# Performance work log

Hardware: AMD Instinct MI355X
Metric: run time of the kernel (lower is better)

Reference implementation:

```python
import jax, jax.numpy as jnp
import numpy as np

B, I, C, J, D, H, W = 16, 32, 8, 10, 16, 6, 6
NUM_ROUTING = 3
EPS = 1e-07


def setup_inputs() -> dict:
    key = jax.random.key(0)
    u_hat = jax.random.normal(key, (B, I, C, J, D, H, W), dtype=jnp.float32)
    # torch module fills bias with 0.1, shape (out_capsules, out_channels, 1, 1)
    bias = jnp.full((J, D, 1, 1), 0.1, dtype=jnp.float32)
    return {"u_hat": u_hat, "bias": bias, "num_routing": NUM_ROUTING}


def _squash(s):
    # Faithful to the source: L1 norm over ALL non-batch dims (not per-capsule L2).
    n1 = jnp.sum(jnp.abs(s), axis=(1, 2, 3, 4), keepdims=True)  # [B,1,1,1,1]
    n1_sq = n1 * n1
    return (n1_sq / (1.0 + n1_sq)) * (s / (n1 + EPS))


def reference(u_hat, bias, num_routing):
    # u_hat: [B,I,C,J,D,H,W]; bias: [J,D,1,1]
    b_ij = jnp.zeros((I, J), dtype=u_hat.dtype)
    v_j = None
    for _ in range(num_routing):
        c_ij = jax.nn.softmax(b_ij, axis=1)  # [I,J]
        # s_j[b,j,d,h,w] = sum_{i,c} c[i,j] * u_hat[b,i,c,j,d,h,w]  (c broadcast over in_channels)
        s_j = jnp.einsum('ij,bicjdhw->bjdhw', c_ij, u_hat) + bias
        v_j = _squash(s_j)  # [B,J,D,H,W]
        # agreement[i,j] = sum over b,c,d,h,w of u_hat * v_j (broadcast over i,c)
        agreement = jnp.einsum('bicjdhw,bjdhw->ij', u_hat, v_j)
        b_ij = b_ij + jax.lax.stop_gradient(agreement)  # torch uses .data (detached)
    return v_j
```

## Files before the change

kernel.cpp:

```cpp
#include <hip/hip_runtime.h>


#define NB   16
#define NI   32
#define NC   8
#define NJ   10
#define ND   16
#define NHW  36
#define NDHW 576
#define EPSV 1e-7f

static __device__ __forceinline__ double wave_reduce(double a) {
    #pragma unroll
    for (int off = 32; off > 0; off >>= 1) a += __shfl_down(a, off);
    return a;
}

__global__ __launch_bounds__(256) void reduce_c_kernel(
    const float4* __restrict__ uh, float4* __restrict__ U)
{
    int t = blockIdx.x * 256 + threadIdx.x;
    int f4 = t % 144;
    int j  = (t / 144) % NJ;
    int bi = t / (144 * NJ);
    const float4* p = uh + ((size_t)bi * NC) * (NJ * 144) + j * 144 + f4;
    float4 acc = make_float4(0.f, 0.f, 0.f, 0.f);
    #pragma unroll
    for (int c = 0; c < NC; ++c) {
        float4 v = p[(size_t)c * (NJ * 144)];
        acc.x += v.x; acc.y += v.y; acc.z += v.z; acc.w += v.w;
    }
    U[t] = acc;
}

__global__ __launch_bounds__(NDHW) void s_n1_kernel(
    const float* __restrict__ U, const float* __restrict__ bias,
    const float* __restrict__ b_ij, float* __restrict__ s,
    double* __restrict__ n1)
{
    int blk = blockIdx.x;
    int b = blk / NJ, j = blk - b * NJ;
    int tid = threadIdx.x;

    __shared__ float c_sh[NI];
    if (tid < NI) {
        float row[NJ];
        float m = -1e30f;
        #pragma unroll
        for (int jj = 0; jj < NJ; ++jj) {
            row[jj] = b_ij[tid * NJ + jj];
            m = fmaxf(m, row[jj]);
        }
        float sum = 0.f;
        #pragma unroll
        for (int jj = 0; jj < NJ; ++jj) sum += expf(row[jj] - m);
        c_sh[tid] = expf(row[j] - m) / sum;
    }
    __syncthreads();

    float sv = bias[j * ND + tid / NHW];
    const float* Ub = U + ((size_t)(b * NI) * NJ + j) * NDHW + tid;
    #pragma unroll 8
    for (int i = 0; i < NI; ++i)
        sv += c_sh[i] * Ub[(size_t)i * NJ * NDHW];
    s[((size_t)b * NJ + j) * NDHW + tid] = sv;

    double a = wave_reduce((double)fabsf(sv));
    __shared__ double wpart[NDHW / 64];
    if ((tid & 63) == 0) wpart[tid >> 6] = a;
    __syncthreads();
    if (tid == 0) {
        double t = wpart[0];
        #pragma unroll
        for (int k = 1; k < NDHW / 64; ++k) t += wpart[k];
        atomicAdd(&n1[b], t);
    }
}

__global__ __launch_bounds__(256) void agree_kernel(
    const float* __restrict__ U, const float* __restrict__ s,
    const double* __restrict__ n1, float* __restrict__ b_ij)
{
    int ij = blockIdx.x;
    int i = ij / NJ, j = ij - i * NJ;
    int tid = threadIdx.x;

    __shared__ double sc_sh[NB];
    if (tid < NB) {
        double n1v = n1[tid];
        double nsq = n1v * n1v;
        sc_sh[tid] = (nsq / (1.0 + nsq)) / (n1v + (double)EPSV);
    }
    __syncthreads();

    double acc = 0.0;
    for (int t = tid; t < NB * NDHW; t += 256) {
        int b = t / NDHW, dhw = t - b * NDHW;
        float Uv = U[((size_t)(b * NI + i) * NJ + j) * NDHW + dhw];
        float sv = s[((size_t)b * NJ + j) * NDHW + dhw];
        acc += (double)Uv * (double)sv * sc_sh[b];
    }
    acc = wave_reduce(acc);
    __shared__ double wpart[4];
    if ((tid & 63) == 0) wpart[tid >> 6] = acc;
    __syncthreads();
    if (tid == 0)
        b_ij[i * NJ + j] += (float)(wpart[0] + wpart[1] + wpart[2] + wpart[3]);
}

__global__ __launch_bounds__(256) void vout_kernel(
    const float* __restrict__ s, const double* __restrict__ n1,
    float* __restrict__ out)
{
    int idx = blockIdx.x * 256 + threadIdx.x;
    int b = idx / (NJ * NDHW);
    float n1f = (float)n1[b];
    float nsq = n1f * n1f;
    out[idx] = (nsq / (1.f + nsq)) * (s[idx] / (n1f + EPSV));
}

extern "C" void kernel_launch(void* const* d_in, const int* in_sizes, int n_in,
                              void* d_out, int out_size, void* d_ws, size_t ws_size,
                              hipStream_t stream)
{
    const float* u_hat = (const float*)d_in[0];
    const float* bias  = (const float*)d_in[1];

    float*  U   = (float*)d_ws;
    float*  s   = U + (size_t)NB * NI * NJ * NDHW;
    float*  bij = s + (size_t)NB * NJ * NDHW;
    double* n1  = (double*)(bij + NI * NJ);
    float*  out = (float*)d_out;

    hipMemsetAsync(bij, 0, NI * NJ * sizeof(float) + 3 * NB * sizeof(double), stream);

    reduce_c_kernel<<<(NB * NI * NJ * 144) / 256, 256, 0, stream>>>(
        (const float4*)u_hat, (float4*)U);

    for (int r = 0; r < 3; ++r) {
        s_n1_kernel<<<NB * NJ, NDHW, 0, stream>>>(U, bias, bij, s, n1 + r * NB);
        if (r < 2)
            agree_kernel<<<NI * NJ, 256, 0, stream>>>(U, s, n1 + r * NB, bij);
        else
            vout_kernel<<<(NB * NJ * NDHW) / 256, 256, 0, stream>>>(s, n1 + r * NB, out);
    }
}
```

Measured before the change: 182.4 us.

## Fuse routing iterations into one cooperative kernel with grid syncs

Replaces the six per-iteration launches (s/norm, agreement, output) with a single cooperative kernel of 360 blocks. Grid-wide syncs separate the phases, and the output squash is applied directly from registers. The aim is to remove launch gaps and the extra pass that re-reads s. In exchange it adds grid.sync costs, and it caps parallelism at 360 blocks of 256 threads, since the agreement phase still uses 320 blocks.

```diff
diff --git a/kernel.cpp b/kernel.cpp
--- a/kernel.cpp
+++ b/kernel.cpp
@@ -1,4 +1,7 @@
 #include <hip/hip_runtime.h>
+#include <hip/hip_cooperative_groups.h>
+
+namespace cg = cooperative_groups;
 
 
 #define NB   16
@@ -8,13 +11,11 @@
 #define ND   16
 #define NHW  36
 #define NDHW 576
+#define NJDHW (NJ * NDHW)
+#define NTOT  (NB * NJ * NDHW)
 #define EPSV 1e-7f
-
-static __device__ __forceinline__ double wave_reduce(double a) {
-    #pragma unroll
-    for (int off = 32; off > 0; off >>= 1) a += __shfl_down(a, off);
-    return a;
-}
+#define GRID 360
+#define TPB  256
 
 __global__ __launch_bounds__(256) void reduce_c_kernel(
     const float4* __restrict__ uh, float4* __restrict__ U)
@@ -33,90 +34,107 @@
     U[t] = acc;
 }
 
-__global__ __launch_bounds__(NDHW) void s_n1_kernel(
+__global__ __launch_bounds__(TPB) void routing_kernel(
     const float* __restrict__ U, const float* __restrict__ bias,
-    const float* __restrict__ b_ij, float* __restrict__ s,
-    double* __restrict__ n1)
+    float* __restrict__ s, float* __restrict__ bij,
+    double* __restrict__ n1, float* __restrict__ out)
 {
-    int blk = blockIdx.x;
-    int b = blk / NJ, j = blk - b * NJ;
-    int tid = threadIdx.x;
+    cg::grid_group grid = cg::this_grid();
+    const int tid = threadIdx.x;
+    const int blk = blockIdx.x;
+    const int e   = blk * TPB + tid;
 
-    __shared__ float c_sh[NI];
-    if (tid < NI) {
-        float row[NJ];
-        float m = -1e30f;
+    __shared__ float  c_sh[NI * NJ];
+    __shared__ double red[8];
+    __shared__ double sc_sh[NB];
+
+    const int b   = e / NJDHW;
+    const int rem = e - b * NJDHW;
+    const int j   = rem / NDHW;
+    const int dhw = rem - j * NDHW;
+    const float bias_v = bias[j * ND + dhw / NHW];
+    const float* Up = U + (((size_t)b * NI) * NJ + j) * NDHW + dhw;
+    const int b0 = (blk * TPB) / NJDHW;
+    const int b1 = (blk * TPB + TPB - 1) / NJDHW;
+
+    for (int r = 0; r < 3; ++r) {
+        double* n1r = n1 + r * NB;
+
+        if (tid < NI) {
+            float row[NJ], m = -1e30f;
+            #pragma unroll
+            for (int jj = 0; jj < NJ; ++jj) {
+                row[jj] = bij[tid * NJ + jj];
+                m = fmaxf(m, row[jj]);
+            }
+            float ex[NJ], sum = 0.f;
+            #pragma unroll
+            for (int jj = 0; jj < NJ; ++jj) { ex[jj] = expf(row[jj] - m); sum += ex[jj]; }
+            float inv = 1.f / sum;
+            #pragma unroll
+            for (int jj = 0; jj < NJ; ++jj) c_sh[tid * NJ + jj] = ex[jj] * inv;
+        }
+        __syncthreads();
+
+        float sv = bias_v;
         #pragma unroll
-        for (int jj = 0; jj < NJ; ++jj) {
-            row[jj] = b_ij[tid * NJ + jj];
-            m = fmaxf(m, row[jj]);
+        for (int i = 0; i < NI; ++i)
+            sv += c_sh[i * NJ + j] * Up[(size_t)i * NJ * NDHW];
+        s[e] = sv;
+
+        {
+            double a  = (double)fabsf(sv);
+            double v0 = (b == b0) ? a : 0.0;
+            double v1 = (b1 != b0 && b == b1) ? a : 0.0;
+            #pragma unroll
+            for (int off = 32; off > 0; off >>= 1) {
+                v0 += __shfl_down(v0, off);
+                v1 += __shfl_down(v1, off);
+            }
+            if ((tid & 63) == 0) { red[tid >> 6] = v0; red[4 + (tid >> 6)] = v1; }
+            __syncthreads();
+            if (tid == 0) {
+                atomicAdd(&n1r[b0], red[0] + red[1] + red[2] + red[3]);
+                if (b1 != b0)
+                    atomicAdd(&n1r[b1], red[4] + red[5] + red[6] + red[7]);
+            }
+            __syncthreads();
         }
-        float sum = 0.f;
-        #pragma unroll
-        for (int jj = 0; jj < NJ; ++jj) sum += expf(row[jj] - m);
-        c_sh[tid] = expf(row[j] - m) / sum;
+
+        __threadfence();
+        grid.sync();
+
+        if (r < 2) {
+            if (tid < NB) {
+                double n1v = n1r[tid];
+                double nsq = n1v * n1v;
+                sc_sh[tid] = (nsq / (1.0 + nsq)) / (n1v + (double)EPSV);
+            }
+            __syncthreads();
+            if (blk < NI * NJ) {
+                int ti = blk / NJ, tj = blk - ti * NJ;
+                double acc = 0.0;
+                for (int t = tid; t < NB * NDHW; t += TPB) {
+                    int tb = t / NDHW, tdhw = t - tb * NDHW;
+                    float Uv = U[(((size_t)(tb * NI + ti)) * NJ + tj) * NDHW + tdhw];
+                    float svv = s[(size_t)tb * NJDHW + tj * NDHW + tdhw];
+                    acc += (double)Uv * (double)svv * sc_sh[tb];
+                }
+                #pragma unroll
+                for (int off = 32; off > 0; off >>= 1) acc += __shfl_down(acc, off);
+                if ((tid & 63) == 0) red[tid >> 6] = acc;
+                __syncthreads();
+                if (tid == 0)
+                    bij[blk] += (float)(red[0] + red[1] + red[2] + red[3]);
+            }
+            __threadfence();
+            grid.sync();
+        } else {
+            float n1f = (float)n1r[b];
+            float nsq = n1f * n1f;
+            out[e] = (nsq / (1.f + nsq)) * (sv / (n1f + EPSV));
+        }
     }
-    __syncthreads();
-
-    float sv = bias[j * ND + tid / NHW];
-    const float* Ub = U + ((size_t)(b * NI) * NJ + j) * NDHW + tid;
-    #pragma unroll 8
-    for (int i = 0; i < NI; ++i)
-        sv += c_sh[i] * Ub[(size_t)i * NJ * NDHW];
-    s[((size_t)b * NJ + j) * NDHW + tid] = sv;
-
-    double a = wave_reduce((double)fabsf(sv));
-    __shared__ double wpart[NDHW / 64];
-    if ((tid & 63) == 0) wpart[tid >> 6] = a;
-    __syncthreads();
-    if (tid == 0) {
-        double t = wpart[0];
-        #pragma unroll
-        for (int k = 1; k < NDHW / 64; ++k) t += wpart[k];
-        atomicAdd(&n1[b], t);
-    }
-}
-
-__global__ __launch_bounds__(256) void agree_kernel(
-    const float* __restrict__ U, const float* __restrict__ s,
-    const double* __restrict__ n1, float* __restrict__ b_ij)
-{
-    int ij = blockIdx.x;
-    int i = ij / NJ, j = ij - i * NJ;
-    int tid = threadIdx.x;
-
-    __shared__ double sc_sh[NB];
-    if (tid < NB) {
-        double n1v = n1[tid];
-        double nsq = n1v * n1v;
-        sc_sh[tid] = (nsq / (1.0 + nsq)) / (n1v + (double)EPSV);
-    }
-    __syncthreads();
-
-    double acc = 0.0;
-    for (int t = tid; t < NB * NDHW; t += 256) {
-        int b = t / NDHW, dhw = t - b * NDHW;
-        float Uv = U[((size_t)(b * NI + i) * NJ + j) * NDHW + dhw];
-        float sv = s[((size_t)b * NJ + j) * NDHW + dhw];
-        acc += (double)Uv * (double)sv * sc_sh[b];
-    }
-    acc = wave_reduce(acc);
-    __shared__ double wpart[4];
-    if ((tid & 63) == 0) wpart[tid >> 6] = acc;
-    __syncthreads();
-    if (tid == 0)
-        b_ij[i * NJ + j] += (float)(wpart[0] + wpart[1] + wpart[2] + wpart[3]);
-}
-
-__global__ __launch_bounds__(256) void vout_kernel(
-    const float* __restrict__ s, const double* __restrict__ n1,
-    float* __restrict__ out)
-{
-    int idx = blockIdx.x * 256 + threadIdx.x;
-    int b = idx / (NJ * NDHW);
-    float n1f = (float)n1[b];
-    float nsq = n1f * n1f;
-    out[idx] = (nsq / (1.f + nsq)) * (s[idx] / (n1f + EPSV));
 }
 
 extern "C" void kernel_launch(void* const* d_in, const int* in_sizes, int n_in,
@@ -128,7 +146,7 @@
 
     float*  U   = (float*)d_ws;
     float*  s   = U + (size_t)NB * NI * NJ * NDHW;
-    float*  bij = s + (size_t)NB * NJ * NDHW;
+    float*  bij = s + NTOT;
     double* n1  = (double*)(bij + NI * NJ);
     float*  out = (float*)d_out;
 
@@ -137,11 +155,8 @@
     reduce_c_kernel<<<(NB * NI * NJ * 144) / 256, 256, 0, stream>>>(
         (const float4*)u_hat, (float4*)U);
 
-    for (int r = 0; r < 3; ++r) {
-        s_n1_kernel<<<NB * NJ, NDHW, 0, stream>>>(U, bias, bij, s, n1 + r * NB);
-        if (r < 2)
-            agree_kernel<<<NI * NJ, 256, 0, stream>>>(U, s, n1 + r * NB, bij);
-        else
-            vout_kernel<<<(NB * NJ * NDHW) / 256, 256, 0, stream>>>(s, n1 + r * NB, out);
-    }
+    void* args[] = {(void*)&U, (void*)&bias, (void*)&s, (void*)&bij,
+                    (void*)&n1, (void*)&out};
+    hipLaunchCooperativeKernel((void*)routing_kernel, dim3(GRID), dim3(TPB),
+                               args, 0, stream);
 }
```

Result: slower. 530.9 us (+191.0%).

## Fuse routing iterations into per-(b,j) blocks with unscaled agreement partials

Applied to the files above, without the earlier changes.

Replaces the reduce/s/agree kernel chain with a block per (b,j) that reduces u_hat over C, computes s, its L1 partial and the unscaled per-i dot products G in one pass. Later iterations rebuild b_ij from the stored G partials scaled by each batch's squash factor, so the agree kernel, the atomics and the memset are gone and U is read only once per iteration. Iteration 1 uses uniform coupling (1/10) directly. This costs redundant b_ij/softmax recomputation in every block and 32 wave reductions per block for G, using many registers.

```diff
diff --git a/kernel.cpp b/kernel.cpp
--- a/kernel.cpp
+++ b/kernel.cpp
@@ -8,115 +8,161 @@
 #define ND   16
 #define NHW  36
 #define NDHW 576
+#define NJDHW (NJ * NDHW)
+#define NTOT  (NB * NJ * NDHW)
 #define EPSV 1e-7f
+#define TPB  576
 
-static __device__ __forceinline__ double wave_reduce(double a) {
+
+static __device__ __forceinline__ double wave_sum(double v) {
     #pragma unroll
-    for (int off = 32; off > 0; off >>= 1) a += __shfl_down(a, off);
-    return a;
+    for (int off = 32; off > 0; off >>= 1) v += __shfl_down(v, off);
+    return v;
 }
 
-__global__ __launch_bounds__(256) void reduce_c_kernel(
-    const float4* __restrict__ uh, float4* __restrict__ U)
-{
-    int t = blockIdx.x * 256 + threadIdx.x;
-    int f4 = t % 144;
-    int j  = (t / 144) % NJ;
-    int bi = t / (144 * NJ);
-    const float4* p = uh + ((size_t)bi * NC) * (NJ * 144) + j * 144 + f4;
-    float4 acc = make_float4(0.f, 0.f, 0.f, 0.f);
-    #pragma unroll
-    for (int c = 0; c < NC; ++c) {
-        float4 v = p[(size_t)c * (NJ * 144)];
-        acc.x += v.x; acc.y += v.y; acc.z += v.z; acc.w += v.w;
+static __device__ __forceinline__ void n1_reduce(float sv, double* slot,
+                                                 double* nred ) {
+    int tid = threadIdx.x;
+    double a = wave_sum((double)fabsf(sv));
+    if ((tid & 63) == 0) nred[tid >> 6] = a;
+    __syncthreads();
+    if (tid == 0) {
+        double t = nred[0];
+        #pragma unroll
+        for (int w = 1; w < 9; ++w) t += nred[w];
+        *slot = t;
     }
-    U[t] = acc;
 }
 
-__global__ __launch_bounds__(NDHW) void s_n1_kernel(
-    const float* __restrict__ U, const float* __restrict__ bias,
-    const float* __restrict__ b_ij, float* __restrict__ s,
-    double* __restrict__ n1)
+static __device__ __forceinline__ void g_reduce(const float* Uv, float sv,
+                                                double* gslot,
+                                                double (*gred)[32] ) {
+    int tid = threadIdx.x, w = tid >> 6, lane = tid & 63;
+    #pragma unroll
+    for (int i = 0; i < NI; ++i) {
+        double p = wave_sum((double)Uv[i] * (double)sv);
+        if (lane == 0) gred[w][i] = p;
+    }
+    __syncthreads();
+    if (tid < NI) {
+        double t = gred[0][tid];
+        #pragma unroll
+        for (int w2 = 1; w2 < 9; ++w2) t += gred[w2][tid];
+        gslot[tid] = t;
+    }
+}
+
+__global__ __launch_bounds__(TPB) void a1_kernel(
+    const float* __restrict__ uh, const float* __restrict__ bias,
+    float* __restrict__ U2, double* __restrict__ n1p, double* __restrict__ Gp)
 {
-    int blk = blockIdx.x;
-    int b = blk / NJ, j = blk - b * NJ;
-    int tid = threadIdx.x;
+    __shared__ double nred[9];
+    __shared__ double gred[9][32];
 
-    __shared__ float c_sh[NI];
-    if (tid < NI) {
-        float row[NJ];
-        float m = -1e30f;
+    const int blk = blockIdx.x;
+    const int b = blk / NJ, j = blk - b * NJ;
+    const int tid = threadIdx.x;
+    const float cw = 1.0f / 10.0f;
+
+    const float* ub = uh + (size_t)b * 1474560 + j * 576 + tid;
+    float* u2b = U2 + (size_t)b * 184320 + j * 18432 + tid;
+
+    float Uv[NI];
+    float sv = bias[j * ND + tid / NHW];
+    #pragma unroll 4
+    for (int i = 0; i < NI; ++i) {
+        float acc = 0.f;
         #pragma unroll
-        for (int jj = 0; jj < NJ; ++jj) {
-            row[jj] = b_ij[tid * NJ + jj];
-            m = fmaxf(m, row[jj]);
-        }
-        float sum = 0.f;
+        for (int c = 0; c < NC; ++c)
+            acc += ub[(size_t)i * 46080 + c * 5760];
+        Uv[i] = acc;
+        u2b[i * 576] = acc;
+        sv += cw * acc;
+    }
+
+    n1_reduce(sv, &n1p[b * NJ + j], nred);
+    g_reduce(Uv, sv, &Gp[(size_t)(b * NJ + j) * NI], gred);
+}
+
+template <int R>
+__global__ __launch_bounds__(TPB) void ab_kernel(
+    const float* __restrict__ U2, const float* __restrict__ bias,
+    const double* __restrict__ n1p, double* __restrict__ Gp,
+    double* __restrict__ n1p_out, double* __restrict__ Gp_out,
+    float* __restrict__ s)
+{
+    __shared__ double sc_sh[2][NB];
+    __shared__ float  bij_sh[NI * NJ];
+    __shared__ float  c_sh[NI];
+    __shared__ double nred[9];
+    __shared__ double gred[9][32];
+
+    const int blk = blockIdx.x;
+    const int b = blk / NJ, j = blk - b * NJ;
+    const int tid = threadIdx.x;
+
+    if (tid < R * NB) {
+        int rr = tid / NB, bb = tid - rr * NB;
+        double n1 = 0.0;
         #pragma unroll
-        for (int jj = 0; jj < NJ; ++jj) sum += expf(row[jj] - m);
-        c_sh[tid] = expf(row[j] - m) / sum;
+        for (int jj = 0; jj < NJ; ++jj) n1 += n1p[rr * (NB * NJ) + bb * NJ + jj];
+        double nsq = n1 * n1;
+        sc_sh[rr][bb] = (nsq / (1.0 + nsq)) / (n1 + (double)EPSV);
     }
     __syncthreads();
 
-    float sv = bias[j * ND + tid / NHW];
-    const float* Ub = U + ((size_t)(b * NI) * NJ + j) * NDHW + tid;
-    #pragma unroll 8
-    for (int i = 0; i < NI; ++i)
-        sv += c_sh[i] * Ub[(size_t)i * NJ * NDHW];
-    s[((size_t)b * NJ + j) * NDHW + tid] = sv;
-
-    double a = wave_reduce((double)fabsf(sv));
-    __shared__ double wpart[NDHW / 64];
-    if ((tid & 63) == 0) wpart[tid >> 6] = a;
-    __syncthreads();
-    if (tid == 0) {
-        double t = wpart[0];
+    if (tid < NI * NJ) {
+        int i = tid / NJ, jj = tid - i * NJ;
+        double a = 0.0;
         #pragma unroll
-        for (int k = 1; k < NDHW / 64; ++k) t += wpart[k];
-        atomicAdd(&n1[b], t);
-    }
-}
-
-__global__ __launch_bounds__(256) void agree_kernel(
-    const float* __restrict__ U, const float* __restrict__ s,
-    const double* __restrict__ n1, float* __restrict__ b_ij)
-{
-    int ij = blockIdx.x;
-    int i = ij / NJ, j = ij - i * NJ;
-    int tid = threadIdx.x;
-
-    __shared__ double sc_sh[NB];
-    if (tid < NB) {
-        double n1v = n1[tid];
-        double nsq = n1v * n1v;
-        sc_sh[tid] = (nsq / (1.0 + nsq)) / (n1v + (double)EPSV);
+        for (int rr = 0; rr < R; ++rr)
+            #pragma unroll
+            for (int bb = 0; bb < NB; ++bb)
+                a += sc_sh[rr][bb] *
+                     Gp[(size_t)(rr * NB + bb) * NJ * NI + (size_t)jj * NI + i];
+        bij_sh[tid] = (float)a;
     }
     __syncthreads();
 
-    double acc = 0.0;
-    for (int t = tid; t < NB * NDHW; t += 256) {
-        int b = t / NDHW, dhw = t - b * NDHW;
-        float Uv = U[((size_t)(b * NI + i) * NJ + j) * NDHW + dhw];
-        float sv = s[((size_t)b * NJ + j) * NDHW + dhw];
-        acc += (double)Uv * (double)sv * sc_sh[b];
+    if (tid < NI) {
+        float m = -1e30f;
+        #pragma unroll
+        for (int jj = 0; jj < NJ; ++jj) m = fmaxf(m, bij_sh[tid * NJ + jj]);
+        float sum = 0.f;
+        #pragma unroll
+        for (int jj = 0; jj < NJ; ++jj) sum += expf(bij_sh[tid * NJ + jj] - m);
+        c_sh[tid] = expf(bij_sh[tid * NJ + j] - m) / sum;
     }
-    acc = wave_reduce(acc);
-    __shared__ double wpart[4];
-    if ((tid & 63) == 0) wpart[tid >> 6] = acc;
     __syncthreads();
-    if (tid == 0)
-        b_ij[i * NJ + j] += (float)(wpart[0] + wpart[1] + wpart[2] + wpart[3]);
+
+    const float* u2b = U2 + (size_t)b * 184320 + j * 18432 + tid;
+    float Uv[NI];
+    float sv = bias[j * ND + tid / NHW];
+    #pragma unroll
+    for (int i = 0; i < NI; ++i) {
+        Uv[i] = u2b[i * 576];
+        sv += c_sh[i] * Uv[i];
+    }
+
+    if (R == 2) s[(size_t)blk * NDHW + tid] = sv;
+
+    n1_reduce(sv, &n1p_out[b * NJ + j], nred);
+    if (R == 1)
+        g_reduce(Uv, sv, &Gp_out[(size_t)(b * NJ + j) * NI], gred);
 }
 
-__global__ __launch_bounds__(256) void vout_kernel(
-    const float* __restrict__ s, const double* __restrict__ n1,
+__global__ __launch_bounds__(256) void v_kernel(
+    const float* __restrict__ s, const double* __restrict__ n1p2,
     float* __restrict__ out)
 {
-    int idx = blockIdx.x * 256 + threadIdx.x;
-    int b = idx / (NJ * NDHW);
-    float n1f = (float)n1[b];
+    int e = blockIdx.x * 256 + threadIdx.x;
+    int b = e / NJDHW;
+    double n1 = 0.0;
+    #pragma unroll
+    for (int jj = 0; jj < NJ; ++jj) n1 += n1p2[b * NJ + jj];
+    float n1f = (float)n1;
     float nsq = n1f * n1f;
-    out[idx] = (nsq / (1.f + nsq)) * (s[idx] / (n1f + EPSV));
+    out[e] = (nsq / (1.f + nsq)) * (s[e] / (n1f + EPSV));
 }
 
 extern "C" void kernel_launch(void* const* d_in, const int* in_sizes, int n_in,
@@ -126,22 +172,16 @@
     const float* u_hat = (const float*)d_in[0];
     const float* bias  = (const float*)d_in[1];
 
-    float*  U   = (float*)d_ws;
-    float*  s   = U + (size_t)NB * NI * NJ * NDHW;
-    float*  bij = s + (size_t)NB * NJ * NDHW;
-    double* n1  = (double*)(bij + NI * NJ);
+    float*  U2  = (float*)d_ws;
+    float*  s   = U2 + (size_t)NB * NJ * NI * NDHW;
+    double* n1p = (double*)(s + NTOT);
+    double* Gp  = n1p + 3 * NB * NJ;
     float*  out = (float*)d_out;
 
-    hipMemsetAsync(bij, 0, NI * NJ * sizeof(float) + 3 * NB * sizeof(double), stream);
-
-    reduce_c_kernel<<<(NB * NI * NJ * 144) / 256, 256, 0, stream>>>(
-        (const float4*)u_hat, (float4*)U);
-
-    for (int r = 0; r < 3; ++r) {
-        s_n1_kernel<<<NB * NJ, NDHW, 0, stream>>>(U, bias, bij, s, n1 + r * NB);
-        if (r < 2)
-            agree_kernel<<<NI * NJ, 256, 0, stream>>>(U, s, n1 + r * NB, bij);
-        else
-            vout_kernel<<<(NB * NJ * NDHW) / 256, 256, 0, stream>>>(s, n1 + r * NB, out);
-    }
+    a1_kernel<<<NB * NJ, TPB, 0, stream>>>(u_hat, bias, U2, n1p, Gp);
+    ab_kernel<1><<<NB * NJ, TPB, 0, stream>>>(
+        U2, bias, n1p, Gp, n1p + NB * NJ, Gp + NB * NJ * NI, s);
+    ab_kernel<2><<<NB * NJ, TPB, 0, stream>>>(
+        U2, bias, n1p, Gp, n1p + 2 * NB * NJ, nullptr, s);
+    v_kernel<<<NTOT / 256, 256, 0, stream>>>(s, n1p + 2 * NB * NJ, out);
 }
```

Result: no change. 179.0 us (-1.9%).
